# Performance work log

Measured on AMD Instinct MI355X. Metric: run time of the kernel, lower is better.

## Reference

```python
import jax, jax.numpy as jnp
import numpy as np

V, E, H = 256, 16, 10
F2, F3, F4 = 3, 4, 5
CONV_OUT = F2 + F3 + F4  # 12


def setup_inputs() -> dict:
    key = jax.random.key(0)
    ks = jax.random.split(key, 9)
    B, SW, SC = 64, 1024, 20
    inputs = jax.random.randint(ks[0], (B, SW, SC), 0, V, dtype=jnp.int32)
    embeddings = jax.random.normal(ks[1], (V, E), jnp.float32) * 0.1
    kernel2 = jax.random.normal(ks[2], (2, E, 1, F2), jnp.float32) * 0.1
    kernel3 = jax.random.normal(ks[3], (3, E, 1, F3), jnp.float32) * 0.1
    kernel4 = jax.random.normal(ks[4], (4, E, 1, F4), jnp.float32) * 0.1
    # tf.contrib.rnn.LSTMCell: single kernel [input+H, 4H] applied to concat([x, h]), bias [4H]
    w_fw = jax.random.normal(ks[5], (CONV_OUT + H, 4 * H), jnp.float32) * 0.1
    b_fw = jnp.zeros((4 * H,), jnp.float32)
    w_bw = jax.random.normal(ks[6], (CONV_OUT + H, 4 * H), jnp.float32) * 0.1
    b_bw = jnp.zeros((4 * H,), jnp.float32)
    return {"inputs": inputs, "embeddings": embeddings, "kernel2": kernel2,
            "kernel3": kernel3, "kernel4": kernel4, "w_fw": w_fw, "b_fw": b_fw,
            "w_bw": w_bw, "b_bw": b_bw}


def _causal_conv(x, kernel):
    # x: [N, SC, E, 1], kernel: [k, E, 1, f]; left-pad char dim by k-1, valid conv collapses E
    k = kernel.shape[0]
    return jax.lax.conv_general_dilated(
        x, kernel, window_strides=(1, 1),
        padding=[(k - 1, 0), (0, 0)],
        dimension_numbers=("NHWC", "HWIO", "NHWC"))  # -> [N, SC, 1, f]


def _lstm_final_h(seq, W, b):
    # seq: [N, T, D]; returns final hidden state [N, H]. tf gate order: i, j, f, o; forget_bias=1.0
    N = seq.shape[0]
    def step(carry, x_t):
        h, c = carry
        z = jnp.concatenate([x_t, h], axis=-1) @ W + b
        i, j, f, o = jnp.split(z, 4, axis=-1)
        c = jax.nn.sigmoid(f + 1.0) * c + jax.nn.sigmoid(i) * jnp.tanh(j)
        h = jax.nn.sigmoid(o) * jnp.tanh(c)
        return (h, c), None
    init = (jnp.zeros((N, H), seq.dtype), jnp.zeros((N, H), seq.dtype))
    (h, _), _ = jax.lax.scan(step, init, jnp.swapaxes(seq, 0, 1))
    return h


def reference(inputs, embeddings, kernel2, kernel3, kernel4, w_fw, b_fw, w_bw, b_bw):
    B, SW, SC = inputs.shape
    enc = embeddings[inputs]                       # [B, SW, SC, E]
    enc = enc.reshape(B * SW, SC, E, 1)            # [N, SC, E, 1]
    c2 = _causal_conv(enc, kernel2)
    c3 = _causal_conv(enc, kernel3)
    c4 = _causal_conv(enc, kernel4)
    c = jnp.concatenate([c2, c3, c4], axis=3)      # [N, SC, 1, 12]
    c = c.reshape(B * SW, SC, CONV_OUT)
    h_fw = _lstm_final_h(c, w_fw, b_fw)            # forward direction
    h_bw = _lstm_final_h(c[:, ::-1, :], w_bw, b_bw)  # backward direction (reversed seq)
    out = jnp.concatenate([h_fw, h_bw], axis=-1)   # [N, 2H]
    return out.reshape(B, SW, 2 * H)
```

## Files before the change

kernel.cpp:

```cpp
#include <hip/hip_runtime.h>

#define SC 20
#define EDIM 16
#define HDIM 10
#define VOCAB 256
#define SENT VOCAB
#define CROW 72
#define XROW 24
#define WAVES 4

typedef _Float16 f16;
typedef __attribute__((ext_vector_type(2))) _Float16 f16x2;
typedef __attribute__((ext_vector_type(8))) _Float16 f16x8;
typedef __attribute__((ext_vector_type(4))) float f32x4;

#if __has_builtin(__builtin_amdgcn_exp2f)
#define EXP2F(x) __builtin_amdgcn_exp2f(x)
#else
#define EXP2F(x) exp2f(x)
#endif
#if __has_builtin(__builtin_amdgcn_rcpf)
#define RCPF(x) __builtin_amdgcn_rcpf(x)
#else
#define RCPF(x) (1.0f / (x))
#endif
#define L2E 1.44269504088896340736f

__device__ __forceinline__ float fast_sig(float x) {
    return RCPF(1.0f + EXP2F(-x * L2E));
}
__device__ __forceinline__ float fast_tanh(float x) {
    float e = EXP2F(x * (2.0f * L2E));
    return 1.0f - 2.0f * RCPF(1.0f + e);
}
__device__ __forceinline__ f16x2 bc2(unsigned u) { return __builtin_bit_cast(f16x2, u); }
__device__ __forceinline__ unsigned bcu(f16x2 v) { return __builtin_bit_cast(unsigned, v); }
__device__ __forceinline__ unsigned pk(float a, float b) {
    f16x2 t = {(f16)a, (f16)b};
    return __builtin_bit_cast(unsigned, t);
}

__global__ __launch_bounds__(256, 1) void cnn_lstm_kernel(
    const int* __restrict__ inp, const float* __restrict__ emb,
    const float* __restrict__ k2, const float* __restrict__ k3,
    const float* __restrict__ k4,
    const float* __restrict__ wfw, const float* __restrict__ bfw,
    const float* __restrict__ wbw, const float* __restrict__ bbw,
    float* __restrict__ out)
{
    __shared__ __align__(16) f16 ctab[(VOCAB + 1) * CROW];
    __shared__ __align__(16) f16 xbuf[WAVES][65][XROW];

    const int tid  = threadIdx.x;
    const int lane = tid & 63;
    const int w    = tid >> 6;
    const int g    = lane >> 4;
    const int c16  = lane & 15;

    {
        float er[EDIM];
        const float4* ep = (const float4*)(emb + tid * EDIM);
        float4 e0 = ep[0], e1 = ep[1], e2 = ep[2], e3 = ep[3];
        er[0] = e0.x; er[1] = e0.y; er[2] = e0.z; er[3] = e0.w;
        er[4] = e1.x; er[5] = e1.y; er[6] = e1.z; er[7] = e1.w;
        er[8] = e2.x; er[9] = e2.y; er[10] = e2.z; er[11] = e2.w;
        er[12] = e3.x; er[13] = e3.y; er[14] = e3.z; er[15] = e3.w;

        #pragma unroll
        for (int dlt = 0; dlt < 4; ++dlt) {
            float o[12];
            #pragma unroll
            for (int f = 0; f < 12; ++f) o[f] = 0.0f;
            const int tap2 = 1 - dlt, tap3 = 2 - dlt, tap4 = 3 - dlt;
            if (tap2 >= 0) {
                #pragma unroll
                for (int e = 0; e < EDIM; ++e) {
                    const float x = er[e];
                    #pragma unroll
                    for (int f = 0; f < 3; ++f) o[f] += x * k2[(tap2 * EDIM + e) * 3 + f];
                }
            }
            if (tap3 >= 0) {
                #pragma unroll
                for (int e = 0; e < EDIM; ++e) {
                    const float x = er[e];
                    #pragma unroll
                    for (int f = 0; f < 4; ++f) o[3 + f] += x * k3[(tap3 * EDIM + e) * 4 + f];
                }
            }
            {
                #pragma unroll
                for (int e = 0; e < EDIM; ++e) {
                    const float x = er[e];
                    #pragma unroll
                    for (int f = 0; f < 5; ++f) o[7 + f] += x * k4[(tap4 * EDIM + e) * 5 + f];
                }
            }
            f16* dst = &ctab[tid * CROW + 16 * dlt];
            uint4 s;
            s.x = pk(o[0], o[1]); s.y = pk(o[2], o[3]);
            s.z = pk(o[4], o[5]); s.w = pk(o[6], o[7]);
            *(uint4*)dst = s;
            *(uint2*)(dst + 8) = make_uint2(pk(o[8], o[9]), pk(o[10], o[11]));
        }
    }
    if (tid < 9) ((uint4*)&ctab[VOCAB * CROW])[tid] = make_uint4(0, 0, 0, 0);
    __syncthreads();

    const int dir   = blockIdx.x >> 8;
    const bool fw   = (dir == 0);
    const int nbase = (blockIdx.x & 255) * 256 + w * 64;
    const int n_seq = nbase + lane;
    const int* inp_n = inp + n_seq * SC;
    const float* Wm = fw ? wfw : wbw;
    const float* Bv = fw ? bfw : bbw;

    f16x8 afr[3];
    #pragma unroll
    for (int mg = 0; mg < 3; ++mg) {
        const int G = 16 * mg + c16;
        const int Q = G >> 2, r = G & 3;
        #pragma unroll
        for (int i = 0; i < 8; ++i) {
            const int kk = 8 * g + i;
            float val = 0.0f;
            if (Q < HDIM) {
                const int lcol = r * HDIM + Q;
                if (kk < 22) val = Wm[kk * 40 + lcol];
                else if (kk == 22) val = Bv[lcol];
            }
            afr[mg][i] = (f16)val;
        }
    }

    {
        f16* xr = &xbuf[w][lane][0];
        *(uint2*)(xr + 12) = make_uint2(0u, 0u);
        *(uint2*)(xr + 16) = make_uint2(0u, 0u);
        *(unsigned*)(xr + 20) = 0u;
        *(unsigned*)(xr + 22) = pk(1.0f, 0.0f);
    }
    if (lane == 0) {
        uint4* zr = (uint4*)&xbuf[w][64][0];
        zr[0] = make_uint4(0, 0, 0, 0);
        zr[1] = make_uint4(0, 0, 0, 0);
        zr[2] = make_uint4(0, 0, 0, 0);
    }

    float creg[4][3], hreg[4][3];
    #pragma unroll
    for (int ms = 0; ms < 4; ++ms)
        #pragma unroll
        for (int mg = 0; mg < 3; ++mg) { creg[ms][mg] = 0.0f; hreg[ms][mg] = 0.0f; }

    int a0, a1, a2, a3;
    if (fw) {
        a0 = inp_n[0]; a1 = SENT; a2 = SENT; a3 = SENT;
    } else {
        a0 = inp_n[SC - 1]; a1 = inp_n[SC - 2]; a2 = inp_n[SC - 3]; a3 = inp_n[SC - 4];
    }

    #pragma unroll 1
    for (int t = 0; t < SC; ++t) {
        const int nidx = fw ? (t + 1) : (SC - 5 - t);
        int an = SENT;
        if ((t < SC - 1) && (nidx >= 0)) an = inp_n[nidx];

        f16x2 xa0, xa1, xa2, xa3, xa4, xa5;
        {
            const f16* p = &ctab[a0 * CROW];
            uint4 P = *(const uint4*)p; uint2 Q = *(const uint2*)(p + 8);
            xa0 = bc2(P.x); xa1 = bc2(P.y); xa2 = bc2(P.z);
            xa3 = bc2(P.w); xa4 = bc2(Q.x); xa5 = bc2(Q.y);
        }
        {
            const f16* p = &ctab[a1 * CROW + 16];
            uint4 P = *(const uint4*)p; uint2 Q = *(const uint2*)(p + 8);
            xa0 += bc2(P.x); xa1 += bc2(P.y); xa2 += bc2(P.z);
            xa3 += bc2(P.w); xa4 += bc2(Q.x); xa5 += bc2(Q.y);
        }
        {
            const f16* p = &ctab[a2 * CROW + 32];
            uint4 P = *(const uint4*)p; uint2 Q = *(const uint2*)(p + 8);
            xa0 += bc2(P.x); xa1 += bc2(P.y); xa2 += bc2(P.z);
            xa3 += bc2(P.w); xa4 += bc2(Q.x); xa5 += bc2(Q.y);
        }
        {
            const f16* p = &ctab[a3 * CROW + 48];
            uint4 P = *(const uint4*)p; uint2 Q = *(const uint2*)(p + 8);
            xa0 += bc2(P.x); xa1 += bc2(P.y); xa2 += bc2(P.z);
            xa3 += bc2(P.w); xa4 += bc2(Q.x); xa5 += bc2(Q.y);
        }

        {
            f16* xr = &xbuf[w][lane][0];
            uint4 W0;
            W0.x = bcu(xa0); W0.y = bcu(xa1); W0.z = bcu(xa2); W0.w = bcu(xa3);
            *(uint4*)xr = W0;
            *(uint2*)(xr + 8) = make_uint2(bcu(xa4), bcu(xa5));
        }
        __builtin_amdgcn_sched_barrier(0);

        f32x4 acc[4][3];
        const f32x4 zero4 = {0.0f, 0.0f, 0.0f, 0.0f};
        #pragma unroll
        for (int ms = 0; ms < 4; ++ms) {
            f16x8 bf = *(const f16x8*)&xbuf[w][16 * ms + c16][8 * g];
            #pragma unroll
            for (int mg = 0; mg < 3; ++mg)
                acc[ms][mg] = __builtin_amdgcn_mfma_f32_16x16x32_f16(afr[mg], bf, zero4, 0, 0, 0);
        }
        __builtin_amdgcn_sched_barrier(0);

        #pragma unroll
        for (int ms = 0; ms < 4; ++ms) {
            #pragma unroll
            for (int mg = 0; mg < 3; ++mg) {
                const f32x4 z = acc[ms][mg];
                const float ij = fast_sig(z[0]) * fast_tanh(z[1]);
                const float fg = fast_sig(z[2] + 1.0f);
                const float og = fast_sig(z[3]);
                const float cc = fg * creg[ms][mg] + ij;
                creg[ms][mg] = cc;
                const float hh = og * fast_tanh(cc);
                hreg[ms][mg] = hh;
                const int Q = 4 * mg + g;
                if (Q < HDIM)
                    xbuf[w][16 * ms + c16][12 + Q] = (f16)hh;
            }
        }
        __builtin_amdgcn_sched_barrier(0);

        if (fw) { a3 = a2; a2 = a1; a1 = a0; a0 = an; }
        else    { a0 = a1; a1 = a2; a2 = a3; a3 = an; }
    }

    #pragma unroll
    for (int ms = 0; ms < 4; ++ms) {
        #pragma unroll
        for (int mg = 0; mg < 3; ++mg) {
            const int Q = 4 * mg + g;
            if (Q < HDIM)
                out[(nbase + 16 * ms + c16) * (2 * HDIM) + dir * HDIM + Q] = hreg[ms][mg];
        }
    }
}

extern "C" void kernel_launch(void* const* d_in, const int* in_sizes, int n_in,
                              void* d_out, int out_size, void* d_ws, size_t ws_size,
                              hipStream_t stream) {
    const int*   inp = (const int*)d_in[0];
    const float* emb = (const float*)d_in[1];
    const float* k2  = (const float*)d_in[2];
    const float* k3  = (const float*)d_in[3];
    const float* k4  = (const float*)d_in[4];
    const float* wfw = (const float*)d_in[5];
    const float* bfw = (const float*)d_in[6];
    const float* wbw = (const float*)d_in[7];
    const float* bbw = (const float*)d_in[8];
    float* out = (float*)d_out;

    cnn_lstm_kernel<<<dim3(512), dim3(256), 0, stream>>>(
        inp, emb, k2, k3, k4, wfw, bfw, wbw, bbw, out);
}
```

Measured before the change: 58.76 us.

## Halve sequences per wave, split lanes into gather/compute halves, shrink LDS table

Each wave now handles 32 sequences instead of 64, and the grid doubles to 1024 blocks with launch bounds allowing 4 blocks per CU. The two half-waves alternate: one half gathers and sums the next step's conv table rows while the MFMAs for the current step run, so the gather latency overlaps compute. The conv lookup table is packed more tightly (56 halves per row, stored as shifted 12-wide segments), which cuts LDS use so more blocks fit per CU. The h writeback is also packed into paired f16 stores, and the output goes out as float2. In exchange, the embedding-to-conv table is rebuilt twice as often across blocks, and the gate row mapping and gather indexing become more complex.

```diff
diff --git a/kernel.cpp b/kernel.cpp
--- a/kernel.cpp
+++ b/kernel.cpp
@@ -5,7 +5,7 @@
 #define HDIM 10
 #define VOCAB 256
 #define SENT VOCAB
-#define CROW 72
+#define CROWH 56
 #define XROW 24
 #define WAVES 4
 
@@ -40,7 +40,33 @@
     return __builtin_bit_cast(unsigned, t);
 }
 
-__global__ __launch_bounds__(256, 1) void cnn_lstm_kernel(
+#define G_ISSUE                                                         \
+    {   const f16* q0 = &ctab[a0 * CROWH];                              \
+        g0a = *(const uint4*)q0;  g0b = *(const uint2*)(q0 + 8);        \
+        const f16* q1 = &ctab[a1 * CROWH + 12];                         \
+        g1a = *(const uint2*)q1;  g1b = *(const uint2*)(q1 + 4);        \
+        g1c = *(const uint2*)(q1 + 8);                                  \
+        const f16* q2 = &ctab[a2 * CROWH + 24];                         \
+        g2a = *(const uint4*)q2;  g2b = *(const uint2*)(q2 + 8);        \
+        const f16* q3 = &ctab[a3 * CROWH + 36];                         \
+        g3a = *(const uint2*)q3;  g3b = *(const uint2*)(q3 + 4);        \
+        g3c = *(const uint2*)(q3 + 8); }
+
+#define G_SUM                                                           \
+    {   f16x2 s0 = bc2(g0a.x) + bc2(g1a.x) + bc2(g2a.x) + bc2(g3a.x);  \
+        f16x2 s1 = bc2(g0a.y) + bc2(g1a.y) + bc2(g2a.y) + bc2(g3a.y);  \
+        f16x2 s2 = bc2(g0a.z) + bc2(g1b.x) + bc2(g2a.z) + bc2(g3b.x);  \
+        f16x2 s3 = bc2(g0a.w) + bc2(g1b.y) + bc2(g2a.w) + bc2(g3b.y);  \
+        f16x2 s4 = bc2(g0b.x) + bc2(g1c.x) + bc2(g2b.x) + bc2(g3c.x);  \
+        f16x2 s5 = bc2(g0b.y) + bc2(g1c.y) + bc2(g2b.y) + bc2(g3c.y);  \
+        xg0 = bcu(s0); xg1 = bcu(s1); xg2 = bcu(s2);                   \
+        xg3 = bcu(s3); xg4 = bcu(s4); xg5 = bcu(s5); }
+
+#define G_ADV                                                           \
+    if (fw) { a3 = a1; a2 = a0; a1 = chload(pp + 1); a0 = chload(pp + 2); pp += 2; } \
+    else    { a0 = a2; a1 = a3; a2 = chload(pp - 4); a3 = chload(pp - 5); pp -= 2; }
+
+__global__ __launch_bounds__(256, 4) void cnn_lstm_kernel(
     const int* __restrict__ inp, const float* __restrict__ emb,
     const float* __restrict__ k2, const float* __restrict__ k3,
     const float* __restrict__ k4,
@@ -48,14 +74,16 @@
     const float* __restrict__ wbw, const float* __restrict__ bbw,
     float* __restrict__ out)
 {
-    __shared__ __align__(16) f16 ctab[(VOCAB + 1) * CROW];
-    __shared__ __align__(16) f16 xbuf[WAVES][65][XROW];
+    __shared__ __align__(16) f16 ctab[(VOCAB + 1) * CROWH];
+    __shared__ __align__(16) f16 xbuf[WAVES][33][XROW];
 
     const int tid  = threadIdx.x;
     const int lane = tid & 63;
     const int w    = tid >> 6;
     const int g    = lane >> 4;
     const int c16  = lane & 15;
+    const int p    = lane >> 5;
+    const int s    = lane & 31;
 
     {
         float er[EDIM];
@@ -66,6 +94,7 @@
         er[8] = e2.x; er[9] = e2.y; er[10] = e2.z; er[11] = e2.w;
         er[12] = e3.x; er[13] = e3.y; er[14] = e3.z; er[15] = e3.w;
 
+        unsigned wd[24];
         #pragma unroll
         for (int dlt = 0; dlt < 4; ++dlt) {
             float o[12];
@@ -96,153 +125,145 @@
                     for (int f = 0; f < 5; ++f) o[7 + f] += x * k4[(tap4 * EDIM + e) * 5 + f];
                 }
             }
-            f16* dst = &ctab[tid * CROW + 16 * dlt];
-            uint4 s;
-            s.x = pk(o[0], o[1]); s.y = pk(o[2], o[3]);
-            s.z = pk(o[4], o[5]); s.w = pk(o[6], o[7]);
-            *(uint4*)dst = s;
-            *(uint2*)(dst + 8) = make_uint2(pk(o[8], o[9]), pk(o[10], o[11]));
-        }
-    }
-    if (tid < 9) ((uint4*)&ctab[VOCAB * CROW])[tid] = make_uint4(0, 0, 0, 0);
-    __syncthreads();
-
-    const int dir   = blockIdx.x >> 8;
+            #pragma unroll
+            for (int k = 0; k < 6; ++k) wd[6 * dlt + k] = pk(o[2 * k], o[2 * k + 1]);
+        }
+        uint4* dst = (uint4*)&ctab[tid * CROWH];
+        #pragma unroll
+        for (int j = 0; j < 6; ++j)
+            dst[j] = make_uint4(wd[4 * j], wd[4 * j + 1], wd[4 * j + 2], wd[4 * j + 3]);
+    }
+    if (tid < 6) ((uint4*)&ctab[SENT * CROWH])[tid] = make_uint4(0, 0, 0, 0);
+
+    const int dir   = blockIdx.x >> 9;
     const bool fw   = (dir == 0);
-    const int nbase = (blockIdx.x & 255) * 256 + w * 64;
-    const int n_seq = nbase + lane;
-    const int* inp_n = inp + n_seq * SC;
+    const int nbase = (blockIdx.x & 511) * 128 + w * 32;
+    const int* inp_s = inp + (nbase + s) * SC;
     const float* Wm = fw ? wfw : wbw;
     const float* Bv = fw ? bfw : bbw;
 
     f16x8 afr[3];
-    #pragma unroll
-    for (int mg = 0; mg < 3; ++mg) {
-        const int G = 16 * mg + c16;
-        const int Q = G >> 2, r = G & 3;
-        #pragma unroll
-        for (int i = 0; i < 8; ++i) {
-            const int kk = 8 * g + i;
-            float val = 0.0f;
-            if (Q < HDIM) {
-                const int lcol = r * HDIM + Q;
-                if (kk < 22) val = Wm[kk * 40 + lcol];
-                else if (kk == 22) val = Bv[lcol];
-            }
-            afr[mg][i] = (f16)val;
-        }
-    }
-
     {
-        f16* xr = &xbuf[w][lane][0];
+        const int qg = c16 >> 2, r = c16 & 3;
+        #pragma unroll
+        for (int mg = 0; mg < 3; ++mg) {
+            const int Lq = (mg == 0) ? 2 * qg : (mg == 1) ? (2 * qg + 1) : (8 + qg);
+            const bool valid = (Lq < HDIM);
+            const int lcol = r * HDIM + Lq;
+            #pragma unroll
+            for (int i = 0; i < 8; ++i) {
+                const int kk = 8 * g + i;
+                float val = 0.0f;
+                if (valid) {
+                    if (kk < 22) val = Wm[kk * 40 + lcol];
+                    else if (kk == 22) val = Bv[lcol];
+                }
+                afr[mg][i] = (f16)val;
+            }
+        }
+    }
+
+    if (p == 0) {
+        f16* xr = &xbuf[w][s][0];
         *(uint2*)(xr + 12) = make_uint2(0u, 0u);
         *(uint2*)(xr + 16) = make_uint2(0u, 0u);
-        *(unsigned*)(xr + 20) = 0u;
-        *(unsigned*)(xr + 22) = pk(1.0f, 0.0f);
+        *(uint2*)(xr + 20) = make_uint2(0u, pk(1.0f, 0.0f));
     }
     if (lane == 0) {
-        uint4* zr = (uint4*)&xbuf[w][64][0];
-        zr[0] = make_uint4(0, 0, 0, 0);
-        zr[1] = make_uint4(0, 0, 0, 0);
-        zr[2] = make_uint4(0, 0, 0, 0);
-    }
-
-    float creg[4][3], hreg[4][3];
+        uint4* jr = (uint4*)&xbuf[w][32][0];
+        jr[0] = make_uint4(0, 0, 0, 0);
+        jr[1] = make_uint4(0, 0, 0, 0);
+        jr[2] = make_uint4(0, 0, 0, 0);
+    }
+    __syncthreads();
+
+    auto chload = [&](int q) -> int {
+        return ((unsigned)q < (unsigned)SC) ? inp_s[q] : SENT;
+    };
+
+    int pp = fw ? p : (SC - 1 - p);
+    int a0 = chload(pp), a1 = chload(pp - 1), a2 = chload(pp - 2), a3 = chload(pp - 3);
+
+    unsigned xg0, xg1, xg2, xg3, xg4, xg5;
+    uint4 g0a, g2a;
+    uint2 g0b, g1a, g1b, g1c, g2b, g3a, g3b, g3c;
+
+    if (p == 0) {
+        G_ISSUE
+        G_SUM
+        f16* xr = &xbuf[w][s][0];
+        *(uint4*)xr = make_uint4(xg0, xg1, xg2, xg3);
+        *(uint2*)(xr + 8) = make_uint2(xg4, xg5);
+        G_ADV
+    }
+
+    float creg[2][3], hreg[2][3];
     #pragma unroll
-    for (int ms = 0; ms < 4; ++ms)
+    for (int ms = 0; ms < 2; ++ms)
         #pragma unroll
         for (int mg = 0; mg < 3; ++mg) { creg[ms][mg] = 0.0f; hreg[ms][mg] = 0.0f; }
 
-    int a0, a1, a2, a3;
-    if (fw) {
-        a0 = inp_n[0]; a1 = SENT; a2 = SENT; a3 = SENT;
-    } else {
-        a0 = inp_n[SC - 1]; a1 = inp_n[SC - 2]; a2 = inp_n[SC - 3]; a3 = inp_n[SC - 4];
-    }
+    const f32x4 zero4 = {0.0f, 0.0f, 0.0f, 0.0f};
 
     #pragma unroll 1
     for (int t = 0; t < SC; ++t) {
-        const int nidx = fw ? (t + 1) : (SC - 5 - t);
-        int an = SENT;
-        if ((t < SC - 1) && (nidx >= 0)) an = inp_n[nidx];
-
-        f16x2 xa0, xa1, xa2, xa3, xa4, xa5;
-        {
-            const f16* p = &ctab[a0 * CROW];
-            uint4 P = *(const uint4*)p; uint2 Q = *(const uint2*)(p + 8);
-            xa0 = bc2(P.x); xa1 = bc2(P.y); xa2 = bc2(P.z);
-            xa3 = bc2(P.w); xa4 = bc2(Q.x); xa5 = bc2(Q.y);
-        }
-        {
-            const f16* p = &ctab[a1 * CROW + 16];
-            uint4 P = *(const uint4*)p; uint2 Q = *(const uint2*)(p + 8);
-            xa0 += bc2(P.x); xa1 += bc2(P.y); xa2 += bc2(P.z);
-            xa3 += bc2(P.w); xa4 += bc2(Q.x); xa5 += bc2(Q.y);
-        }
-        {
-            const f16* p = &ctab[a2 * CROW + 32];
-            uint4 P = *(const uint4*)p; uint2 Q = *(const uint2*)(p + 8);
-            xa0 += bc2(P.x); xa1 += bc2(P.y); xa2 += bc2(P.z);
-            xa3 += bc2(P.w); xa4 += bc2(Q.x); xa5 += bc2(Q.y);
-        }
-        {
-            const f16* p = &ctab[a3 * CROW + 48];
-            uint4 P = *(const uint4*)p; uint2 Q = *(const uint2*)(p + 8);
-            xa0 += bc2(P.x); xa1 += bc2(P.y); xa2 += bc2(P.z);
-            xa3 += bc2(P.w); xa4 += bc2(Q.x); xa5 += bc2(Q.y);
-        }
-
-        {
-            f16* xr = &xbuf[w][lane][0];
-            uint4 W0;
-            W0.x = bcu(xa0); W0.y = bcu(xa1); W0.z = bcu(xa2); W0.w = bcu(xa3);
-            *(uint4*)xr = W0;
-            *(uint2*)(xr + 8) = make_uint2(bcu(xa4), bcu(xa5));
-        }
-        __builtin_amdgcn_sched_barrier(0);
-
-        f32x4 acc[4][3];
-        const f32x4 zero4 = {0.0f, 0.0f, 0.0f, 0.0f};
-        #pragma unroll
-        for (int ms = 0; ms < 4; ++ms) {
-            f16x8 bf = *(const f16x8*)&xbuf[w][16 * ms + c16][8 * g];
-            #pragma unroll
-            for (int mg = 0; mg < 3; ++mg)
-                acc[ms][mg] = __builtin_amdgcn_mfma_f32_16x16x32_f16(afr[mg], bf, zero4, 0, 0, 0);
-        }
-        __builtin_amdgcn_sched_barrier(0);
-
-        #pragma unroll
-        for (int ms = 0; ms < 4; ++ms) {
+        const bool iswriter = (p == (t & 1));
+
+        if (t > 0 && iswriter) {
+            f16* xr = &xbuf[w][s][0];
+            *(uint4*)xr = make_uint4(xg0, xg1, xg2, xg3);
+            *(uint2*)(xr + 8) = make_uint2(xg4, xg5);
+        }
+
+        f16x8 bf0 = *(const f16x8*)&xbuf[w][c16][8 * g];
+        f16x8 bf1 = *(const f16x8*)&xbuf[w][16 + c16][8 * g];
+        __builtin_amdgcn_sched_barrier(0);
+
+        const bool dogather = (!iswriter) && (t < SC - 1);
+        if (dogather) {
+            G_ISSUE
+            G_ADV
+        }
+        __builtin_amdgcn_sched_barrier(0);
+
+        f32x4 acc[2][3];
+        #pragma unroll
+        for (int mg = 0; mg < 3; ++mg) {
+            acc[0][mg] = __builtin_amdgcn_mfma_f32_16x16x32_f16(afr[mg], bf0, zero4, 0, 0, 0);
+            acc[1][mg] = __builtin_amdgcn_mfma_f32_16x16x32_f16(afr[mg], bf1, zero4, 0, 0, 0);
+        }
+        __builtin_amdgcn_sched_barrier(0);
+
+        if (dogather) {
+            G_SUM
+        }
+
+        #pragma unroll
+        for (int ms = 0; ms < 2; ++ms) {
             #pragma unroll
             for (int mg = 0; mg < 3; ++mg) {
                 const f32x4 z = acc[ms][mg];
                 const float ij = fast_sig(z[0]) * fast_tanh(z[1]);
                 const float fg = fast_sig(z[2] + 1.0f);
                 const float og = fast_sig(z[3]);
-                const float cc = fg * creg[ms][mg] + ij;
-                creg[ms][mg] = cc;
-                const float hh = og * fast_tanh(cc);
-                hreg[ms][mg] = hh;
-                const int Q = 4 * mg + g;
-                if (Q < HDIM)
-                    xbuf[w][16 * ms + c16][12 + Q] = (f16)hh;
-            }
-        }
-        __builtin_amdgcn_sched_barrier(0);
-
-        if (fw) { a3 = a2; a2 = a1; a1 = a0; a0 = an; }
-        else    { a0 = a1; a1 = a2; a2 = a3; a3 = an; }
+                creg[ms][mg] = fg * creg[ms][mg] + ij;
+                hreg[ms][mg] = og * fast_tanh(creg[ms][mg]);
+            }
+            f16* xr = &xbuf[w][16 * ms + c16][0];
+            *(unsigned*)(xr + 12 + 2 * g) = pk(hreg[ms][0], hreg[ms][1]);
+            if (g < 2) xr[20 + g] = (f16)hreg[ms][2];
+        }
+        __builtin_amdgcn_sched_barrier(0);
     }
 
     #pragma unroll
-    for (int ms = 0; ms < 4; ++ms) {
-        #pragma unroll
-        for (int mg = 0; mg < 3; ++mg) {
-            const int Q = 4 * mg + g;
-            if (Q < HDIM)
-                out[(nbase + 16 * ms + c16) * (2 * HDIM) + dir * HDIM + Q] = hreg[ms][mg];
-        }
+    for (int ms = 0; ms < 2; ++ms) {
+        const int n = nbase + 16 * ms + c16;
+        float2 hv;
+        hv.x = hreg[ms][0];
+        hv.y = hreg[ms][1];
+        *(float2*)&out[n * (2 * HDIM) + dir * HDIM + 2 * g] = hv;
+        if (g < 2) out[n * (2 * HDIM) + dir * HDIM + 8 + g] = hreg[ms][2];
     }
 }
 
@@ -260,6 +281,6 @@
     const float* bbw = (const float*)d_in[8];
     float* out = (float*)d_out;
 
-    cnn_lstm_kernel<<<dim3(512), dim3(256), 0, stream>>>(
+    cnn_lstm_kernel<<<dim3(1024), dim3(256), 0, stream>>>(
         inp, emb, k2, k3, k4, wfw, bfw, wbw, bbw, out);
 }
```

Result: faster. 57.41 us (-2.3%).
